# Kernel tuning notes

Hardware: AMD Instinct MI355X
Metric: run time of the kernel (lower is better)

## Reference

```python
import jax, jax.numpy as jnp
import numpy as np

DIM = 1024
N_HEADS = 16
HEAD_DIM = DIM // N_HEADS


def setup_inputs() -> dict:
    key = jax.random.key(0)
    k1, k2, k3 = jax.random.split(key, 3)
    x = jax.random.normal(k1, (1, 4096, DIM), dtype=jnp.float32)
    # nn.Linear weights stored as [out, in]; y = x @ W.T
    w_qkv = jax.random.normal(k2, (3 * DIM, DIM), dtype=jnp.float32) * (DIM ** -0.5)
    w_o = jax.random.normal(k3, (DIM, DIM), dtype=jnp.float32) * (DIM ** -0.5)
    return {"x": x, "w_qkv": w_qkv, "w_o": w_o}


def reference(x, w_qkv, w_o):
    b, s, _ = x.shape
    qkv = jnp.einsum('bsd,ed->bse', x, w_qkv)  # [b, s, 3*dim]
    qkv = qkv.reshape(b, s, 3, N_HEADS, HEAD_DIM)
    qkv = jnp.transpose(qkv, (2, 0, 3, 1, 4))  # [3, b, h, s, hd]
    q, k, v = qkv[0], qkv[1], qkv[2]
    scale = HEAD_DIM ** -0.5
    scores = jnp.einsum('bhqd,bhkd->bhqk', q, k) * scale  # full O(N^2) scores
    attn = jax.nn.softmax(scores, axis=-1)
    out = jnp.einsum('bhqk,bhkd->bhqd', attn, v)
    out = jnp.transpose(out, (0, 2, 1, 3)).reshape(b, s, DIM)
    return jnp.einsum('bsd,ed->bse', out, w_o)
```

## Files before the change

### kernel.cpp

```cpp
#include <hip/hip_runtime.h>

typedef __bf16 bf16x8 __attribute__((ext_vector_type(8)));
typedef float f32x4 __attribute__((ext_vector_type(4)));
typedef unsigned short ushort_t;
typedef unsigned int uint_t;

constexpr int S = 4096, DMODEL = 1024, NH = 16, HD = 64;
#define QSCALE 0.18033688011112042f

#if __has_builtin(__builtin_amdgcn_exp2f)
#define EXP2(x) __builtin_amdgcn_exp2f(x)
#else
#define EXP2(x) exp2f(x)
#endif

__device__ inline ushort_t f2bf(float f) {
  uint_t u = __builtin_bit_cast(uint_t, f);
  u = u + 0x7FFFu + ((u >> 16) & 1u);
  return (ushort_t)(u >> 16);
}

__device__ inline ushort_t f2bf_hw(float f) {
  __bf16 h = (__bf16)f;
  return __builtin_bit_cast(ushort_t, h);
}

__device__ inline void gl2lds16(const ushort_t* g, ushort_t* l) {
  __builtin_amdgcn_global_load_lds(
      (const __attribute__((address_space(1))) unsigned int*)g,
      (__attribute__((address_space(3))) unsigned int*)l, 16, 0, 0);
}

__global__ __launch_bounds__(256) void cvt_f32_bf16(const float* __restrict__ in,
                                                    ushort_t* __restrict__ out, int n4) {
  int i = blockIdx.x * 256 + threadIdx.x;
  if (i >= n4) return;
  float4 f = reinterpret_cast<const float4*>(in)[i];
  ushort4 o;
  o.x = f2bf(f.x); o.y = f2bf(f.y); o.z = f2bf(f.z); o.w = f2bf(f.w);
  reinterpret_cast<ushort4*>(out)[i] = o;
}

template <int EPI>
__global__ __launch_bounds__(256) void gemm_bt(const ushort_t* __restrict__ A,
                                               const ushort_t* __restrict__ B,
                                               int M, int N, int K,
                                               float* __restrict__ Cf,
                                               ushort_t* __restrict__ qb,
                                               ushort_t* __restrict__ kb,
                                               ushort_t* __restrict__ vtb) {
  __shared__ ushort_t sA[128 * 64];
  __shared__ ushort_t sB[128 * 64];
  const int t = threadIdx.x;
  const int lane = t & 63, w = t >> 6;
  const int wr = w >> 1, wc = w & 1;
  const int rA0 = blockIdx.y * 128, rB0 = blockIdx.x * 128;

  f32x4 acc[4][4];
#pragma unroll
  for (int m = 0; m < 4; ++m)
#pragma unroll
    for (int n = 0; n < 4; ++n) acc[m][n] = (f32x4){0.f, 0.f, 0.f, 0.f};

  const int srow = t >> 3;
  const int scol = (t & 7) * 8;
  const int ldsbase = w * 512;

  for (int k0 = 0; k0 < K; k0 += 64) {
#pragma unroll
    for (int i = 0; i < 4; ++i) {
      int r = i * 32 + srow;
      int kc = scol ^ ((r & 7) << 3);
      gl2lds16(&A[(size_t)(rA0 + r) * K + k0 + kc], &sA[i * 2048 + ldsbase]);
    }
#pragma unroll
    for (int i = 0; i < 4; ++i) {
      int r = i * 32 + srow;
      int kc = scol ^ ((r & 7) << 3);
      gl2lds16(&B[(size_t)(rB0 + r) * K + k0 + kc], &sB[i * 2048 + ldsbase]);
    }
    __syncthreads();
#pragma unroll
    for (int ks = 0; ks < 2; ++ks) {
      const int kk = ks * 32 + (lane >> 4) * 8;
      bf16x8 af[4], bfr[4];
#pragma unroll
      for (int m = 0; m < 4; ++m) {
        int row = wr * 64 + m * 16 + (lane & 15);
        af[m] = *(const bf16x8*)&sA[row * 64 + (kk ^ ((row & 7) << 3))];
      }
#pragma unroll
      for (int n = 0; n < 4; ++n) {
        int row = wc * 64 + n * 16 + (lane & 15);
        bfr[n] = *(const bf16x8*)&sB[row * 64 + (kk ^ ((row & 7) << 3))];
      }
#pragma unroll
      for (int m = 0; m < 4; ++m)
#pragma unroll
        for (int n = 0; n < 4; ++n)
          acc[m][n] = __builtin_amdgcn_mfma_f32_16x16x32_bf16(af[m], bfr[n], acc[m][n], 0, 0, 0);
    }
    __syncthreads();
  }

#pragma unroll
  for (int m = 0; m < 4; ++m)
#pragma unroll
    for (int n = 0; n < 4; ++n)
#pragma unroll
      for (int r = 0; r < 4; ++r) {
        int row = rA0 + wr * 64 + m * 16 + (lane >> 4) * 4 + r;
        int col = rB0 + wc * 64 + n * 16 + (lane & 15);
        float v = acc[m][n][r];
        if constexpr (EPI == 0) {
          Cf[(size_t)row * N + col] = v;
        } else {
          int t3 = col >> 10, h = (col >> 6) & 15, d = col & 63;
          if (t3 == 0)      qb[((size_t)h * S + row) * HD + d] = f2bf_hw(v * QSCALE);
          else if (t3 == 1) kb[((size_t)h * S + row) * HD + d] = f2bf_hw(v);
          else              vtb[((size_t)h * HD + d) * S + row] = f2bf_hw(v);
        }
      }
}

__global__ __launch_bounds__(512) void attn_fwd(const ushort_t* __restrict__ qb,
                                                const ushort_t* __restrict__ kb,
                                                const ushort_t* __restrict__ vtb,
                                                ushort_t* __restrict__ aob) {
  __shared__ ushort_t sK[2][64 * 64];
  __shared__ ushort_t sV[2][64 * 64];
  __shared__ ushort_t sP[8][16 * 64];
  const int t = threadIdx.x, lane = t & 63, w = t >> 6;
  const int h = blockIdx.y;
  const int q0 = blockIdx.x * 128;
  const ushort_t* qh = qb + (size_t)h * S * HD;
  const ushort_t* kh = kb + (size_t)h * S * HD;
  const ushort_t* vh = vtb + (size_t)h * HD * S;

  bf16x8 qf[2];
  {
    int qr = q0 + w * 16 + (lane & 15);
    const ushort_t* p = &qh[(size_t)qr * HD + (lane >> 4) * 8];
    qf[0] = *(const bf16x8*)p;
    qf[1] = *(const bf16x8*)(p + 32);
  }
  f32x4 acc[4];
#pragma unroll
  for (int n = 0; n < 4; ++n) acc[n] = (f32x4){0.f, 0.f, 0.f, 0.f};
  float lsum[4] = {0.f, 0.f, 0.f, 0.f};

  const int srow = t >> 3;
  const int scol = (t & 7) * 8;
  const int kc = scol ^ ((srow & 7) << 3);
  const int ldsbase = w * 512;
  const int kk0 = (lane >> 4) * 8;

  auto stage = [&](int buf, int kv0) {
    gl2lds16(&kh[(size_t)(kv0 + srow) * HD + kc], &sK[buf][ldsbase]);
    gl2lds16(&vh[(size_t)srow * S + kv0 + kc], &sV[buf][ldsbase]);
  };

  constexpr int NT = S / 64;
  stage(0, 0);
  __syncthreads();

  for (int ti = 0; ti < NT; ++ti) {
    const int buf = ti & 1;
    if (ti + 1 < NT) stage(buf ^ 1, (ti + 1) * 64);

    f32x4 sc[4];
    __builtin_amdgcn_s_setprio(1);
#pragma unroll
    for (int nt = 0; nt < 4; ++nt) {
      sc[nt] = (f32x4){0.f, 0.f, 0.f, 0.f};
      int row = nt * 16 + (lane & 15);
#pragma unroll
      for (int ks = 0; ks < 2; ++ks) {
        int kk = ks * 32 + kk0;
        bf16x8 kf = *(const bf16x8*)&sK[buf][row * 64 + (kk ^ ((row & 7) << 3))];
        sc[nt] = __builtin_amdgcn_mfma_f32_16x16x32_bf16(qf[ks], kf, sc[nt], 0, 0, 0);
      }
    }
    __builtin_amdgcn_s_setprio(0);

    float p[4][4];
#pragma unroll
    for (int r = 0; r < 4; ++r) {
      float ps = 0.f;
#pragma unroll
      for (int nt = 0; nt < 4; ++nt) {
        float pv = EXP2(sc[nt][r]);
        p[nt][r] = pv;
        ps += pv;
      }
      lsum[r] += ps;
    }
    const int prow_base = (lane >> 4) * 4;
#pragma unroll
    for (int nt = 0; nt < 4; ++nt) {
      int col = nt * 16 + (lane & 15);
#pragma unroll
      for (int r = 0; r < 4; ++r) {
        int row = prow_base + r;
        sP[w][row * 64 + (col ^ ((row & 7) << 3))] = f2bf_hw(p[nt][r]);
      }
    }
    bf16x8 pf[2];
    {
      int row = lane & 15;
#pragma unroll
      for (int ks = 0; ks < 2; ++ks) {
        int kk = ks * 32 + kk0;
        pf[ks] = *(const bf16x8*)&sP[w][row * 64 + (kk ^ ((row & 7) << 3))];
      }
    }
    __builtin_amdgcn_s_setprio(1);
#pragma unroll
    for (int nt = 0; nt < 4; ++nt) {
      int row = nt * 16 + (lane & 15);
#pragma unroll
      for (int ks = 0; ks < 2; ++ks) {
        int kk = ks * 32 + kk0;
        bf16x8 vf = *(const bf16x8*)&sV[buf][row * 64 + (kk ^ ((row & 7) << 3))];
        acc[nt] = __builtin_amdgcn_mfma_f32_16x16x32_bf16(pf[ks], vf, acc[nt], 0, 0, 0);
      }
    }
    __builtin_amdgcn_s_setprio(0);
    __syncthreads();
  }
  float linv[4];
#pragma unroll
  for (int r = 0; r < 4; ++r) {
    float l = lsum[r];
    l += __shfl_xor(l, 1);
    l += __shfl_xor(l, 2);
    l += __shfl_xor(l, 4);
    l += __shfl_xor(l, 8);
    linv[r] = 1.0f / l;
  }
#pragma unroll
  for (int nt = 0; nt < 4; ++nt)
#pragma unroll
    for (int r = 0; r < 4; ++r) {
      int row = q0 + w * 16 + (lane >> 4) * 4 + r;
      int col = h * HD + nt * 16 + (lane & 15);
      aob[(size_t)row * DMODEL + col] = f2bf_hw(acc[nt][r] * linv[r]);
    }
}

extern "C" void kernel_launch(void* const* d_in, const int* in_sizes, int n_in,
                              void* d_out, int out_size, void* d_ws, size_t ws_size,
                              hipStream_t stream) {
  const float* x = (const float*)d_in[0];
  const float* wqkv = (const float*)d_in[1];
  const float* wo = (const float*)d_in[2];
  float* out = (float*)d_out;
  char* ws = (char*)d_ws;
  const size_t MB = 1024ull * 1024ull;
  ushort_t* xb  = (ushort_t*)(ws);
  ushort_t* wqb = (ushort_t*)(ws + 8 * MB);
  ushort_t* wob = (ushort_t*)(ws + 14 * MB);
  ushort_t* qb  = (ushort_t*)(ws + 16 * MB);
  ushort_t* kb  = (ushort_t*)(ws + 24 * MB);
  ushort_t* vtb = (ushort_t*)(ws + 32 * MB);
  ushort_t* aob = (ushort_t*)(ws + 40 * MB);

  cvt_f32_bf16<<<(S * DMODEL / 4 + 255) / 256, 256, 0, stream>>>(x, xb, S * DMODEL / 4);
  cvt_f32_bf16<<<(3 * DMODEL * DMODEL / 4 + 255) / 256, 256, 0, stream>>>(wqkv, wqb, 3 * DMODEL * DMODEL / 4);
  cvt_f32_bf16<<<(DMODEL * DMODEL / 4 + 255) / 256, 256, 0, stream>>>(wo, wob, DMODEL * DMODEL / 4);

  dim3 g1(3 * DMODEL / 128, S / 128);
  gemm_bt<1><<<g1, 256, 0, stream>>>(xb, wqb, S, 3 * DMODEL, DMODEL, nullptr, qb, kb, vtb);

  dim3 ga(S / 128, NH);
  attn_fwd<<<ga, 512, 0, stream>>>(qb, kb, vtb, aob);

  dim3 g2(DMODEL / 128, S / 128);
  gemm_bt<0><<<g2, 256, 0, stream>>>(aob, wob, S, DMODEL, DMODEL, out, nullptr, nullptr, nullptr);
}
```

Before: 183.0 us.

## Triple-buffer attention K/V staging and use narrower tiles for output projection

The attention kernel moves from double to triple buffering of K/V tiles in LDS. It waits on explicit vmcnt counts with raw s_barrier instead of __syncthreads, so loads run two tiles ahead. Separately, the output projection GEMM gets a 128x64-tile kernel, doubling the block count (to 512) to fill more CUs on a 4096x1024 output. Risks include the extra LDS footprint lowering occupancy, and the hand-written waitcnt depending on the exact number of outstanding loads per stage.

```diff
diff --git a/kernel.cpp b/kernel.cpp
--- a/kernel.cpp
+++ b/kernel.cpp
@@ -123,12 +123,82 @@
       }
 }
 
+__global__ __launch_bounds__(256) void gemm_bt_n64(const ushort_t* __restrict__ A,
+                                                   const ushort_t* __restrict__ B,
+                                                   int M, int N, int K,
+                                                   float* __restrict__ Cf) {
+  __shared__ ushort_t sA[128 * 64];
+  __shared__ ushort_t sB[64 * 64];
+  const int t = threadIdx.x;
+  const int lane = t & 63, w = t >> 6;
+  const int wr = w >> 1, wc = w & 1;
+  const int rA0 = blockIdx.y * 128, rB0 = blockIdx.x * 64;
+
+  f32x4 acc[4][2];
+#pragma unroll
+  for (int m = 0; m < 4; ++m)
+#pragma unroll
+    for (int n = 0; n < 2; ++n) acc[m][n] = (f32x4){0.f, 0.f, 0.f, 0.f};
+
+  const int srow = t >> 3;
+  const int scol = (t & 7) * 8;
+  const int ldsbase = w * 512;
+
+  for (int k0 = 0; k0 < K; k0 += 64) {
+#pragma unroll
+    for (int i = 0; i < 4; ++i) {
+      int r = i * 32 + srow;
+      int kc = scol ^ ((r & 7) << 3);
+      gl2lds16(&A[(size_t)(rA0 + r) * K + k0 + kc], &sA[i * 2048 + ldsbase]);
+    }
+#pragma unroll
+    for (int i = 0; i < 2; ++i) {
+      int r = i * 32 + srow;
+      int kc = scol ^ ((r & 7) << 3);
+      gl2lds16(&B[(size_t)(rB0 + r) * K + k0 + kc], &sB[i * 2048 + ldsbase]);
+    }
+    __syncthreads();
+#pragma unroll
+    for (int ks = 0; ks < 2; ++ks) {
+      const int kk = ks * 32 + (lane >> 4) * 8;
+      bf16x8 af[4], bfr[2];
+#pragma unroll
+      for (int m = 0; m < 4; ++m) {
+        int row = wr * 64 + m * 16 + (lane & 15);
+        af[m] = *(const bf16x8*)&sA[row * 64 + (kk ^ ((row & 7) << 3))];
+      }
+#pragma unroll
+      for (int n = 0; n < 2; ++n) {
+        int row = wc * 32 + n * 16 + (lane & 15);
+        bfr[n] = *(const bf16x8*)&sB[row * 64 + (kk ^ ((row & 7) << 3))];
+      }
+#pragma unroll
+      for (int m = 0; m < 4; ++m)
+#pragma unroll
+        for (int n = 0; n < 2; ++n)
+          acc[m][n] = __builtin_amdgcn_mfma_f32_16x16x32_bf16(af[m], bfr[n], acc[m][n], 0, 0, 0);
+    }
+    __syncthreads();
+  }
+
+#pragma unroll
+  for (int m = 0; m < 4; ++m)
+#pragma unroll
+    for (int n = 0; n < 2; ++n)
+#pragma unroll
+      for (int r = 0; r < 4; ++r) {
+        int row = rA0 + wr * 64 + m * 16 + (lane >> 4) * 4 + r;
+        int col = rB0 + wc * 32 + n * 16 + (lane & 15);
+        Cf[(size_t)row * N + col] = acc[m][n][r];
+      }
+}
+
 __global__ __launch_bounds__(512) void attn_fwd(const ushort_t* __restrict__ qb,
                                                 const ushort_t* __restrict__ kb,
                                                 const ushort_t* __restrict__ vtb,
                                                 ushort_t* __restrict__ aob) {
-  __shared__ ushort_t sK[2][64 * 64];
-  __shared__ ushort_t sV[2][64 * 64];
+  __shared__ ushort_t sK[3][64 * 64];
+  __shared__ ushort_t sV[3][64 * 64];
   __shared__ ushort_t sP[8][16 * 64];
   const int t = threadIdx.x, lane = t & 63, w = t >> 6;
   const int h = blockIdx.y;
@@ -162,11 +232,23 @@
 
   constexpr int NT = S / 64;
   stage(0, 0);
-  __syncthreads();
+  stage(1, 64);
 
   for (int ti = 0; ti < NT; ++ti) {
-    const int buf = ti & 1;
-    if (ti + 1 < NT) stage(buf ^ 1, (ti + 1) * 64);
+    const int buf = ti % 3;
+    if (ti + 2 < NT) {
+      stage((ti + 2) % 3, (ti + 2) * 64);
+      asm volatile("s_waitcnt vmcnt(4)" ::: "memory");
+    } else if (ti + 1 < NT) {
+      asm volatile("s_waitcnt vmcnt(2)" ::: "memory");
+    } else {
+      asm volatile("s_waitcnt vmcnt(0)" ::: "memory");
+    }
+    __builtin_amdgcn_sched_barrier(0);
+    __builtin_amdgcn_s_barrier();
+
+    const ushort_t* Kb = &sK[buf][0];
+    const ushort_t* Vb = &sV[buf][0];
 
     f32x4 sc[4];
     __builtin_amdgcn_s_setprio(1);
@@ -177,7 +259,7 @@
 #pragma unroll
       for (int ks = 0; ks < 2; ++ks) {
         int kk = ks * 32 + kk0;
-        bf16x8 kf = *(const bf16x8*)&sK[buf][row * 64 + (kk ^ ((row & 7) << 3))];
+        bf16x8 kf = *(const bf16x8*)&Kb[row * 64 + (kk ^ ((row & 7) << 3))];
         sc[nt] = __builtin_amdgcn_mfma_f32_16x16x32_bf16(qf[ks], kf, sc[nt], 0, 0, 0);
       }
     }
@@ -221,12 +303,12 @@
 #pragma unroll
       for (int ks = 0; ks < 2; ++ks) {
         int kk = ks * 32 + kk0;
-        bf16x8 vf = *(const bf16x8*)&sV[buf][row * 64 + (kk ^ ((row & 7) << 3))];
+        bf16x8 vf = *(const bf16x8*)&Vb[row * 64 + (kk ^ ((row & 7) << 3))];
         acc[nt] = __builtin_amdgcn_mfma_f32_16x16x32_bf16(pf[ks], vf, acc[nt], 0, 0, 0);
       }
     }
     __builtin_amdgcn_s_setprio(0);
-    __syncthreads();
+    __builtin_amdgcn_s_barrier();
   }
   float linv[4];
 #pragma unroll
@@ -275,6 +357,6 @@
   dim3 ga(S / 128, NH);
   attn_fwd<<<ga, 512, 0, stream>>>(qb, kb, vtb, aob);
 
-  dim3 g2(DMODEL / 128, S / 128);
-  gemm_bt<0><<<g2, 256, 0, stream>>>(aob, wob, S, DMODEL, DMODEL, out, nullptr, nullptr, nullptr);
-}
+  dim3 g2(DMODEL / 64, S / 128);
+  gemm_bt_n64<<<g2, 256, 0, stream>>>(aob, wob, S, DMODEL, DMODEL, out);
+}
```

After: 177.4 us. -3.0%, faster.
